# Kernel tuning notes

Measured on AMD Instinct MI355X. Metric: run time of the kernel, lower is better.

## Reference

```python
import jax, jax.numpy as jnp
import numpy as np

N_NODES = 100000
N_EDGES = 3200000
N_GRAPHS = 1000
F_IN = 3
H = 64


def setup_inputs() -> dict:
    key = jax.random.key(0)
    ks = jax.random.split(key, 12)
    x = jax.random.normal(ks[0], (N_NODES, F_IN), dtype=jnp.float32)
    edge_index = jax.random.randint(ks[1], (2, N_EDGES), 0, N_NODES, dtype=jnp.int64)
    batch = jnp.sort(jax.random.randint(ks[2], (N_NODES,), 0, N_GRAPHS, dtype=jnp.int64))
    def lin(k, fan_in, fan_out):
        bound = 1.0 / np.sqrt(fan_in)
        return jax.random.uniform(k, (fan_in, fan_out), jnp.float32, -bound, bound)
    return {
        "x": x,
        "edge_index": edge_index,
        "batch": batch,
        "eps1": jax.random.uniform(ks[3], (), jnp.float32),
        "eps2": jax.random.uniform(ks[4], (), jnp.float32),
        "eps3": jax.random.uniform(ks[5], (), jnp.float32),
        "W1": lin(ks[6], F_IN, H), "b1": jnp.zeros((H,), jnp.float32),
        "W2": lin(ks[7], H, H),    "b2": jnp.zeros((H,), jnp.float32),
        "W3": lin(ks[8], H, H),    "b3": jnp.zeros((H,), jnp.float32),
        "Wf1": lin(ks[9], H, 10),  "bf1": jnp.zeros((10,), jnp.float32),
        "Wf2": lin(ks[10], 10, 1), "bf2": jnp.zeros((1,), jnp.float32),
    }


def gin_conv(x, src, dst, eps, W, b):
    # GIN: out = nn((1+eps)*x + sum_{j in N(i)} x_j)
    agg = jax.ops.segment_sum(x[src], dst, num_segments=N_NODES)
    h = (1.0 + eps) * x + agg
    return h @ W + b


def reference(x, edge_index, batch, eps1, eps2, eps3, W1, b1, W2, b2, W3, b3, Wf1, bf1, Wf2, bf2):
    src, dst = edge_index[0], edge_index[1]
    h = jax.nn.relu(gin_conv(x, src, dst, eps1, W1, b1))
    h = jax.nn.relu(gin_conv(h, src, dst, eps2, W2, b2))
    h = jax.nn.relu(gin_conv(h, src, dst, eps3, W3, b3))
    # global mean pool over graphs
    sums = jax.ops.segment_sum(h, batch, num_segments=N_GRAPHS)
    counts = jax.ops.segment_sum(jnp.ones((N_NODES, 1), h.dtype), batch, num_segments=N_GRAPHS)
    pooled = sums / jnp.maximum(counts, 1.0)
    out = jax.nn.relu(pooled @ Wf1 + bf1)
    return out @ Wf2 + bf2
```

## Files before the change

kernel.cpp:

```cpp
#include <hip/hip_runtime.h>

#define N_NODES  100000
#define N_EDGES  3200000
#define N_GRAPHS 1000
#define HDIM     64

#define BUCK_LOG 8
#define BUCK_SZ  256
#define NBUCK    ((N_NODES + BUCK_SZ - 1) / BUCK_SZ)
#define BIN_T    256
#define BIN_E    16
#define BIN_CHUNK (BIN_T * BIN_E)
#define CLUS_CAP 12288

typedef __attribute__((ext_vector_type(8))) short short8;
typedef __attribute__((ext_vector_type(4))) float f32x4;
typedef __attribute__((ext_vector_type(4))) int   int4v;


__device__ inline unsigned short f2bf(float v) {
    unsigned int b; __builtin_memcpy(&b, &v, 4);
    return (unsigned short)((b + 0x7FFFu + ((b >> 16) & 1u)) >> 16);
}
__device__ inline float bf2f(unsigned short u) {
    return __uint_as_float(((unsigned int)u) << 16);
}
__device__ inline void sth(unsigned short* p, float v) { *p = f2bf(v); }
__device__ inline float bflo(unsigned int d) { return __uint_as_float(d << 16); }
__device__ inline float bfhi(unsigned int d) { return __uint_as_float(d & 0xFFFF0000u); }

__device__ inline int clampi(int v, int lo, int hi) {
    return v < lo ? lo : (v > hi ? hi : v);
}


__global__ void k_zero(int* __restrict__ p, int n) {
    int i = blockIdx.x * blockDim.x + threadIdx.x;
    if (i < n) p[i] = 0;
}


__global__ __launch_bounds__(BIN_T) void k_bcount(
        const int* __restrict__ ei, int* __restrict__ btot) {
    __shared__ int hist[NBUCK];
    for (int i = threadIdx.x; i < NBUCK; i += BIN_T) hist[i] = 0;
    __syncthreads();
    int e0 = blockIdx.x * BIN_CHUNK + threadIdx.x * BIN_E;
    if (e0 + BIN_E <= N_EDGES) {
        const int4v* d4 = (const int4v*)(ei + N_EDGES);
        #pragma unroll
        for (int q = 0; q < 4; ++q) {
            int4v dv = d4[(e0 >> 2) + q];
            #pragma unroll
            for (int j = 0; j < 4; ++j) {
                int d = clampi(dv[j], 0, N_NODES - 1);
                atomicAdd(&hist[d >> BUCK_LOG], 1);
            }
        }
    } else {
        for (int k = 0; k < BIN_E; ++k) {
            int e = e0 + k;
            if (e < N_EDGES) {
                int d = clampi(ei[N_EDGES + e], 0, N_NODES - 1);
                atomicAdd(&hist[d >> BUCK_LOG], 1);
            }
        }
    }
    __syncthreads();
    for (int i = threadIdx.x; i < NBUCK; i += BIN_T) {
        int c = hist[i];
        if (c) atomicAdd(&btot[i], c);
    }
}

__global__ void k_bscan(const int* __restrict__ btot, int* __restrict__ bbase,
                        int* __restrict__ gcur, int* __restrict__ off) {
    __shared__ int s[NBUCK + 1];
    int t = threadIdx.x;
    if (t < NBUCK) s[t] = btot[t];
    __syncthreads();
    if (t == 0) {
        int run = 0;
        for (int i = 0; i < NBUCK; ++i) { int x = s[i]; s[i] = run; run += x; }
        s[NBUCK] = run;
    }
    __syncthreads();
    if (t <= NBUCK) bbase[t] = s[t];
    if (t < NBUCK)  gcur[t] = s[t];
    if (t == 0)     off[N_NODES] = s[NBUCK];
}

__global__ __launch_bounds__(BIN_T) void k_bin(
        const int* __restrict__ ei, int* __restrict__ gcur,
        unsigned* __restrict__ pairs) {
    __shared__ int hist[NBUCK];
    __shared__ int base[NBUCK];
    for (int i = threadIdx.x; i < NBUCK; i += BIN_T) hist[i] = 0;
    __syncthreads();
    int e0 = blockIdx.x * BIN_CHUNK + threadIdx.x * BIN_E;
    int d[BIN_E], s[BIN_E];
    if (e0 + BIN_E <= N_EDGES) {
        const int4v* s4 = (const int4v*)ei;
        const int4v* d4 = (const int4v*)(ei + N_EDGES);
        #pragma unroll
        for (int q = 0; q < 4; ++q) {
            int4v dv = d4[(e0 >> 2) + q];
            int4v sv = s4[(e0 >> 2) + q];
            #pragma unroll
            for (int j = 0; j < 4; ++j) {
                d[q * 4 + j] = clampi(dv[j], 0, N_NODES - 1);
                s[q * 4 + j] = clampi(sv[j], 0, N_NODES - 1);
            }
        }
        #pragma unroll
        for (int k = 0; k < BIN_E; ++k) atomicAdd(&hist[d[k] >> BUCK_LOG], 1);
    } else {
        for (int k = 0; k < BIN_E; ++k) {
            int e = e0 + k;
            bool v = e < N_EDGES;
            d[k] = v ? clampi(ei[N_EDGES + e], 0, N_NODES - 1) : -1;
            s[k] = v ? clampi(ei[e], 0, N_NODES - 1) : 0;
            if (v) atomicAdd(&hist[d[k] >> BUCK_LOG], 1);
        }
    }
    __syncthreads();
    for (int i = threadIdx.x; i < NBUCK; i += BIN_T) {
        int c = hist[i];
        base[i] = c ? atomicAdd(&gcur[i], c) : 0;
        hist[i] = 0;
    }
    __syncthreads();
    #pragma unroll
    for (int k = 0; k < BIN_E; ++k) {
        if (d[k] >= 0) {
            int b = d[k] >> BUCK_LOG;
            int r = atomicAdd(&hist[b], 1);
            pairs[base[b] + r] = ((unsigned)(d[k] & (BUCK_SZ - 1)) << 24) | (unsigned)s[k];
        }
    }
}

__global__ __launch_bounds__(512) void k_cluster(
        const unsigned* __restrict__ pairs, const int* __restrict__ bbase,
        int* __restrict__ off, int* __restrict__ adj) {
    __shared__ int ladj[CLUS_CAP];
    __shared__ int lcur[BUCK_SZ];
    __shared__ int lsc[BUCK_SZ];
    int b  = blockIdx.x;
    int lo = b * BUCK_SZ;
    int nn = N_NODES - lo; if (nn > BUCK_SZ) nn = BUCK_SZ;
    int e0 = bbase[b], e1 = bbase[b + 1];
    int cnt = e1 - e0;
    if (threadIdx.x < BUCK_SZ) lcur[threadIdx.x] = 0;
    __syncthreads();
    for (int i = threadIdx.x; i < cnt; i += 512) {
        unsigned p = pairs[e0 + i];
        atomicAdd(&lcur[p >> 24], 1);
    }
    __syncthreads();
    int v = 0;
    if (threadIdx.x < BUCK_SZ) { v = lcur[threadIdx.x]; lsc[threadIdx.x] = v; }
    __syncthreads();
    #pragma unroll
    for (int d = 1; d < BUCK_SZ; d <<= 1) {
        int add = 0;
        if (threadIdx.x < BUCK_SZ && threadIdx.x >= d) add = lsc[threadIdx.x - d];
        __syncthreads();
        if (threadIdx.x < BUCK_SZ) lsc[threadIdx.x] += add;
        __syncthreads();
    }
    if (threadIdx.x < BUCK_SZ) {
        int exc = lsc[threadIdx.x] - v;
        if (threadIdx.x < nn) off[lo + threadIdx.x] = e0 + exc;
        lcur[threadIdx.x] = exc;
    }
    __syncthreads();
    if (cnt <= CLUS_CAP) {
        for (int i = threadIdx.x; i < cnt; i += 512) {
            unsigned p = pairs[e0 + i];
            int pos = atomicAdd(&lcur[p >> 24], 1);
            ladj[pos] = (int)(p & 0xFFFFFFu);
        }
        __syncthreads();
        for (int i = threadIdx.x; i < cnt; i += 512) adj[e0 + i] = ladj[i];
    } else {
        for (int i = threadIdx.x; i < cnt; i += 512) {
            unsigned p = pairs[e0 + i];
            int pos = atomicAdd(&lcur[p >> 24], 1);
            adj[e0 + pos] = (int)(p & 0xFFFFFFu);
        }
    }
}


__global__ __launch_bounds__(256) void k_layer1(
        const float* __restrict__ x, const int* __restrict__ off,
        const int* __restrict__ adj, const float* __restrict__ epsp,
        const float* __restrict__ W1, const float* __restrict__ b1,
        unsigned short* __restrict__ hout) {
    int wid  = (blockIdx.x * blockDim.x + threadIdx.x) >> 6;
    int lane = threadIdx.x & 63;
    if (wid >= N_NODES) return;
    int o0 = off[wid], o1 = off[wid + 1];
    float a0 = 0.f, a1 = 0.f, a2 = 0.f;
    for (int e = o0 + lane; e < o1; e += 64) {
        int s = adj[e];
        a0 += x[s * 3 + 0];
        a1 += x[s * 3 + 1];
        a2 += x[s * 3 + 2];
    }
    #pragma unroll
    for (int d = 32; d; d >>= 1) {
        a0 += __shfl_xor(a0, d);
        a1 += __shfl_xor(a1, d);
        a2 += __shfl_xor(a2, d);
    }
    float ep = 1.0f + epsp[0];
    float s0 = ep * x[wid * 3 + 0] + a0;
    float s1 = ep * x[wid * 3 + 1] + a1;
    float s2 = ep * x[wid * 3 + 2] + a2;
    float o = b1[lane] + s0 * W1[lane] + s1 * W1[64 + lane] + s2 * W1[128 + lane];
    sth(&hout[(size_t)wid * 64 + lane], fmaxf(o, 0.f));
}


__global__ __launch_bounds__(256) void k_gemm(
        const unsigned short* __restrict__ hin, const float* __restrict__ W,
        unsigned short* __restrict__ Y) {
    int lane = threadIdx.x & 63;
    int r = lane & 15;
    int g = lane >> 4;
    int wave   = blockIdx.x * (blockDim.x >> 6) + (threadIdx.x >> 6);
    int nwaves = gridDim.x * (blockDim.x >> 6);

    short8 bh[2][4], bl[2][4];
    #pragma unroll
    for (int s = 0; s < 2; ++s) {
        #pragma unroll
        for (int t = 0; t < 4; ++t) {
            short8 hv, lv;
            #pragma unroll
            for (int i = 0; i < 8; ++i) {
                int k = s * 32 + g * 8 + i;
                int n = t * 16 + r;
                float w = W[k * 64 + n];
                unsigned short wh = f2bf(w);
                float whf = bf2f(wh);
                hv[i] = (short)wh;
                lv[i] = (short)f2bf(w - whf);
            }
            bh[s][t] = hv; bl[s][t] = lv;
        }
    }

    const int NT = N_NODES / 16;
    for (int mt = wave; mt < NT; mt += nwaves) {
        const unsigned short* arow = hin + (size_t)(mt * 16 + r) * 64;
        short8 a0 = *(const short8*)(arow + g * 8);
        short8 a1 = *(const short8*)(arow + 32 + g * 8);
        #pragma unroll
        for (int t = 0; t < 4; ++t) {
            f32x4 acc = {0.f, 0.f, 0.f, 0.f};
            acc = __builtin_amdgcn_mfma_f32_16x16x32_bf16(a0, bh[0][t], acc, 0, 0, 0);
            acc = __builtin_amdgcn_mfma_f32_16x16x32_bf16(a0, bl[0][t], acc, 0, 0, 0);
            acc = __builtin_amdgcn_mfma_f32_16x16x32_bf16(a1, bh[1][t], acc, 0, 0, 0);
            acc = __builtin_amdgcn_mfma_f32_16x16x32_bf16(a1, bl[1][t], acc, 0, 0, 0);
            #pragma unroll
            for (int j = 0; j < 4; ++j) {
                sth(&Y[(size_t)(mt * 16 + g * 4 + j) * 64 + t * 16 + r], acc[j]);
            }
        }
    }
}


__device__ inline void gather_node(
        const uint2* __restrict__ h2, const int* __restrict__ off,
        const int* __restrict__ adj, int node, int sl, int g4,
        float& a0, float& a1, float& a2, float& a3) {
    int o0 = off[node], o1 = off[node + 1];
    int deg = o1 - o0;
    int nchunk = (deg + 15) >> 4;
    for (int c = 0; c < nchunk; ++c) {
        int pos = o0 + (c << 4) + sl;
        int posc = pos < o1 ? pos : (o1 - 1);
        int idxv = adj[posc];
        int rem = deg - (c << 4);
        #pragma unroll
        for (int half = 0; half < 2; ++half) {
            uint2 dd[8];
            #pragma unroll
            for (int i = 0; i < 8; ++i) {
                int k = half * 8 + i;
                int s = __shfl(idxv, (g4 << 4) + k);
                dd[i] = h2[(size_t)s * 16 + sl];
            }
            #pragma unroll
            for (int i = 0; i < 8; ++i) {
                int k = half * 8 + i;
                int ok = k < rem;
                unsigned int lo = ok ? dd[i].x : 0u;
                unsigned int hc = ok ? dd[i].y : 0u;
                a0 += bflo(lo); a1 += bfhi(lo);
                a2 += bflo(hc); a3 += bfhi(hc);
            }
            if (rem <= 8) break;
        }
    }
}

__global__ __launch_bounds__(512) void k_gather(
        const unsigned short* __restrict__ Y, const int* __restrict__ off,
        const int* __restrict__ adj, const float* __restrict__ epsp,
        const float* __restrict__ b, unsigned short* __restrict__ hout) {
    int tid  = blockIdx.x * 512 + threadIdx.x;
    int node = tid >> 4;
    if (node >= N_NODES) return;
    int sl = threadIdx.x & 15;
    int g4 = (threadIdx.x >> 4) & 3;
    const uint2* h2 = (const uint2*)Y;
    float a0 = 0.f, a1 = 0.f, a2 = 0.f, a3 = 0.f;
    gather_node(h2, off, adj, node, sl, g4, a0, a1, a2, a3);
    uint2 ds = h2[(size_t)node * 16 + sl];
    float ep = 1.0f + epsp[0];
    a0 = fmaxf(a0 + ep * bflo(ds.x) + b[4 * sl + 0], 0.f);
    a1 = fmaxf(a1 + ep * bfhi(ds.x) + b[4 * sl + 1], 0.f);
    a2 = fmaxf(a2 + ep * bflo(ds.y) + b[4 * sl + 2], 0.f);
    a3 = fmaxf(a3 + ep * bfhi(ds.y) + b[4 * sl + 3], 0.f);
    uint2 o;
    o.x = (unsigned int)f2bf(a0) | ((unsigned int)f2bf(a1) << 16);
    o.y = (unsigned int)f2bf(a2) | ((unsigned int)f2bf(a3) << 16);
    ((uint2*)hout)[(size_t)node * 16 + sl] = o;
}

__global__ __launch_bounds__(512) void k_gather_pool(
        const unsigned short* __restrict__ Y, const int* __restrict__ off,
        const int* __restrict__ adj, const float* __restrict__ epsp,
        const float* __restrict__ b, const int* __restrict__ batch,
        float* __restrict__ pooled, int* __restrict__ cnt) {
    __shared__ float sacc[8 * 64];
    __shared__ int   scnt[8];
    for (int i = threadIdx.x; i < 8 * 64; i += 512) sacc[i] = 0.f;
    if (threadIdx.x < 8) scnt[threadIdx.x] = 0;
    __syncthreads();

    int tid  = blockIdx.x * 512 + threadIdx.x;
    int node = tid >> 4;
    int sl = threadIdx.x & 15;
    int g4 = (threadIdx.x >> 4) & 3;
    int g0 = clampi(batch[clampi(blockIdx.x * 32, 0, N_NODES - 1)], 0, N_GRAPHS - 1);

    if (node < N_NODES) {
        const uint2* h2 = (const uint2*)Y;
        float a0 = 0.f, a1 = 0.f, a2 = 0.f, a3 = 0.f;
        gather_node(h2, off, adj, node, sl, g4, a0, a1, a2, a3);
        uint2 ds = h2[(size_t)node * 16 + sl];
        float ep = 1.0f + epsp[0];
        a0 = fmaxf(a0 + ep * bflo(ds.x) + b[4 * sl + 0], 0.f);
        a1 = fmaxf(a1 + ep * bfhi(ds.x) + b[4 * sl + 1], 0.f);
        a2 = fmaxf(a2 + ep * bflo(ds.y) + b[4 * sl + 2], 0.f);
        a3 = fmaxf(a3 + ep * bfhi(ds.y) + b[4 * sl + 3], 0.f);
        int g  = clampi(batch[node], 0, N_GRAPHS - 1);
        int og = g - g0;
        if (og >= 0 && og < 8) {
            atomicAdd(&sacc[og * 64 + 4 * sl + 0], a0);
            atomicAdd(&sacc[og * 64 + 4 * sl + 1], a1);
            atomicAdd(&sacc[og * 64 + 4 * sl + 2], a2);
            atomicAdd(&sacc[og * 64 + 4 * sl + 3], a3);
            if (sl == 0) atomicAdd(&scnt[og], 1);
        } else {
            atomicAdd(&pooled[g * 64 + 4 * sl + 0], a0);
            atomicAdd(&pooled[g * 64 + 4 * sl + 1], a1);
            atomicAdd(&pooled[g * 64 + 4 * sl + 2], a2);
            atomicAdd(&pooled[g * 64 + 4 * sl + 3], a3);
            if (sl == 0) atomicAdd(&cnt[g], 1);
        }
    }
    __syncthreads();
    int w = threadIdx.x >> 6;
    int lane = threadIdx.x & 63;
    if (w < 8) {
        int c = scnt[w];
        if (c > 0) {
            atomicAdd(&pooled[(g0 + w) * 64 + lane], sacc[w * 64 + lane]);
            if (lane == 0) atomicAdd(&cnt[g0 + w], c);
        }
    }
}


__global__ __launch_bounds__(256) void k_head(
        const float* __restrict__ pooled, const int* __restrict__ cnt,
        const float* __restrict__ Wf1, const float* __restrict__ bf1,
        const float* __restrict__ Wf2, const float* __restrict__ bf2,
        float* __restrict__ out) {
    int g = blockIdx.x * blockDim.x + threadIdx.x;
    if (g >= N_GRAPHS) return;
    float inv = 1.0f / fmaxf((float)cnt[g], 1.0f);
    float p[64];
    #pragma unroll
    for (int k = 0; k < 64; ++k) p[k] = pooled[g * 64 + k] * inv;
    float o = bf2[0];
    #pragma unroll
    for (int j = 0; j < 10; ++j) {
        float s = bf1[j];
        #pragma unroll
        for (int k = 0; k < 64; ++k) s += p[k] * Wf1[k * 10 + j];
        o += fmaxf(s, 0.f) * Wf2[j];
    }
    out[g] = o;
}


extern "C" void kernel_launch(void* const* d_in, const int* in_sizes, int n_in,
                              void* d_out, int out_size, void* d_ws, size_t ws_size,
                              hipStream_t stream) {
    const float* x     = (const float*)d_in[0];
    const int*   ei    = (const int*)d_in[1];
    const int*   batch = (const int*)d_in[2];
    const float* eps1 = (const float*)d_in[3];
    const float* eps2 = (const float*)d_in[4];
    const float* eps3 = (const float*)d_in[5];
    const float* W1 = (const float*)d_in[6];
    const float* b1 = (const float*)d_in[7];
    const float* W2 = (const float*)d_in[8];
    const float* b2 = (const float*)d_in[9];
    const float* W3 = (const float*)d_in[10];
    const float* b3 = (const float*)d_in[11];
    const float* Wf1 = (const float*)d_in[12];
    const float* bf1 = (const float*)d_in[13];
    const float* Wf2 = (const float*)d_in[14];
    const float* bf2 = (const float*)d_in[15];
    float* out = (float*)d_out;

    const size_t H64 = (size_t)N_NODES * HDIM;

    char* base = (char*)d_ws;
    unsigned short* hA = (unsigned short*)base;
    unsigned short* hB = (unsigned short*)(base + H64 * 2);
    unsigned* pairs = (unsigned*)base;
    char* q = base + 2 * H64 * 2;
    float* pooled = (float*)q;            q += 64000ull * 4;
    int*   cnt    = (int*)q;              q += 1000ull * 4;
    int*   off    = (int*)q;              q += 100004ull * 4;
    int*   btot   = (int*)q;              q += 512ull * 4;
    int*   bbase  = (int*)q;              q += 512ull * 4;
    int*   gcur   = (int*)q;              q += 512ull * 4;
    int*   adj    = (int*)q;

    const int TB = 256;
    k_zero<<<(65000 + TB - 1) / TB, TB, 0, stream>>>((int*)pooled, 65000);
    k_zero<<<2, TB, 0, stream>>>(btot, NBUCK);

    const int BINB = (N_EDGES + BIN_CHUNK - 1) / BIN_CHUNK;
    k_bcount<<<BINB, BIN_T, 0, stream>>>(ei, btot);
    k_bscan<<<1, 512, 0, stream>>>(btot, bbase, gcur, off);
    k_bin<<<BINB, BIN_T, 0, stream>>>(ei, gcur, pairs);
    k_cluster<<<NBUCK, 512, 0, stream>>>(pairs, bbase, off, adj);

    const int L1_BLOCKS = (int)((H64 + TB - 1) / TB);
    const int GB = (N_NODES * 16 + 511) / 512;

    k_layer1<<<L1_BLOCKS, TB, 0, stream>>>(x, off, adj, eps1, W1, b1, hA);
    k_gemm<<<256, 256, 0, stream>>>(hA, W2, hB);
    k_gather<<<GB, 512, 0, stream>>>(hB, off, adj, eps2, b2, hA);
    k_gemm<<<256, 256, 0, stream>>>(hA, W3, hB);
    k_gather_pool<<<GB, 512, 0, stream>>>(hB, off, adj, eps3, b3, batch, pooled, cnt);

    k_head<<<(N_GRAPHS + TB - 1) / TB, TB, 0, stream>>>(pooled, cnt, Wf1, bf1, Wf2, bf2, out);
}
```

Before: 266.5 us.

## Use fixed-capacity edge buckets and pad adjacency lists to chunks of 16

```diff
diff --git a/kernel.cpp b/kernel.cpp
--- a/kernel.cpp
+++ b/kernel.cpp
@@ -8,6 +8,7 @@
 #define BUCK_LOG 8
 #define BUCK_SZ  256
 #define NBUCK    ((N_NODES + BUCK_SZ - 1) / BUCK_SZ)
+#define CAP      16384
 #define BIN_T    256
 #define BIN_E    16
 #define BIN_CHUNK (BIN_T * BIN_E)
@@ -39,56 +40,18 @@
     if (i < n) p[i] = 0;
 }
 
-
-__global__ __launch_bounds__(BIN_T) void k_bcount(
-        const int* __restrict__ ei, int* __restrict__ btot) {
-    __shared__ int hist[NBUCK];
-    for (int i = threadIdx.x; i < NBUCK; i += BIN_T) hist[i] = 0;
-    __syncthreads();
-    int e0 = blockIdx.x * BIN_CHUNK + threadIdx.x * BIN_E;
-    if (e0 + BIN_E <= N_EDGES) {
-        const int4v* d4 = (const int4v*)(ei + N_EDGES);
-        #pragma unroll
-        for (int q = 0; q < 4; ++q) {
-            int4v dv = d4[(e0 >> 2) + q];
-            #pragma unroll
-            for (int j = 0; j < 4; ++j) {
-                int d = clampi(dv[j], 0, N_NODES - 1);
-                atomicAdd(&hist[d >> BUCK_LOG], 1);
-            }
-        }
-    } else {
-        for (int k = 0; k < BIN_E; ++k) {
-            int e = e0 + k;
-            if (e < N_EDGES) {
-                int d = clampi(ei[N_EDGES + e], 0, N_NODES - 1);
-                atomicAdd(&hist[d >> BUCK_LOG], 1);
-            }
-        }
-    }
-    __syncthreads();
-    for (int i = threadIdx.x; i < NBUCK; i += BIN_T) {
-        int c = hist[i];
-        if (c) atomicAdd(&btot[i], c);
-    }
-}
-
-__global__ void k_bscan(const int* __restrict__ btot, int* __restrict__ bbase,
-                        int* __restrict__ gcur, int* __restrict__ off) {
-    __shared__ int s[NBUCK + 1];
+__global__ void k_curinit(int* __restrict__ gcur) {
+    int b = blockIdx.x * blockDim.x + threadIdx.x;
+    if (b < NBUCK) gcur[b] = b * CAP;
+}
+
+__global__ void k_zrow(uint2* __restrict__ hA, uint2* __restrict__ hB) {
     int t = threadIdx.x;
-    if (t < NBUCK) s[t] = btot[t];
-    __syncthreads();
-    if (t == 0) {
-        int run = 0;
-        for (int i = 0; i < NBUCK; ++i) { int x = s[i]; s[i] = run; run += x; }
-        s[NBUCK] = run;
-    }
-    __syncthreads();
-    if (t <= NBUCK) bbase[t] = s[t];
-    if (t < NBUCK)  gcur[t] = s[t];
-    if (t == 0)     off[N_NODES] = s[NBUCK];
-}
+    uint2 z; z.x = 0u; z.y = 0u;
+    if (t < 16)       hA[(size_t)N_NODES * 16 + t] = z;
+    else if (t < 32)  hB[(size_t)N_NODES * 16 + (t - 16)] = z;
+}
+
 
 __global__ __launch_bounds__(BIN_T) void k_bin(
         const int* __restrict__ ei, int* __restrict__ gcur,
@@ -133,81 +96,98 @@
     #pragma unroll
     for (int k = 0; k < BIN_E; ++k) {
         if (d[k] >= 0) {
-            int b = d[k] >> BUCK_LOG;
-            int r = atomicAdd(&hist[b], 1);
-            pairs[base[b] + r] = ((unsigned)(d[k] & (BUCK_SZ - 1)) << 24) | (unsigned)s[k];
+            int bk = d[k] >> BUCK_LOG;
+            int r = atomicAdd(&hist[bk], 1);
+            int idx = base[bk] + r;
+            if (idx < (bk + 1) * CAP)
+                pairs[idx] = ((unsigned)(d[k] & (BUCK_SZ - 1)) << 24) | (unsigned)s[k];
         }
     }
 }
 
 __global__ __launch_bounds__(512) void k_cluster(
-        const unsigned* __restrict__ pairs, const int* __restrict__ bbase,
-        int* __restrict__ off, int* __restrict__ adj) {
+        const unsigned* __restrict__ pairs, const int* __restrict__ gcur,
+        int* __restrict__ poff, int* __restrict__ adj) {
     __shared__ int ladj[CLUS_CAP];
     __shared__ int lcur[BUCK_SZ];
     __shared__ int lsc[BUCK_SZ];
+    __shared__ int ptot;
     int b  = blockIdx.x;
     int lo = b * BUCK_SZ;
     int nn = N_NODES - lo; if (nn > BUCK_SZ) nn = BUCK_SZ;
-    int e0 = bbase[b], e1 = bbase[b + 1];
-    int cnt = e1 - e0;
-    if (threadIdx.x < BUCK_SZ) lcur[threadIdx.x] = 0;
-    __syncthreads();
-    for (int i = threadIdx.x; i < cnt; i += 512) {
-        unsigned p = pairs[e0 + i];
-        atomicAdd(&lcur[p >> 24], 1);
-    }
-    __syncthreads();
-    int v = 0;
-    if (threadIdx.x < BUCK_SZ) { v = lcur[threadIdx.x]; lsc[threadIdx.x] = v; }
+    int e0 = b * CAP;
+    int cnt = gcur[b] - e0; if (cnt > CAP) cnt = CAP;
+    int t = threadIdx.x;
+    if (t < BUCK_SZ) lcur[t] = 0;
+    __syncthreads();
+    for (int i = t; i < cnt; i += 512) atomicAdd(&lcur[pairs[e0 + i] >> 24], 1);
+    __syncthreads();
+    int deg = 0, pdeg = 0;
+    if (t < BUCK_SZ) {
+        deg  = lcur[t];
+        pdeg = (deg + 15) & ~15;
+        if (pdeg > 2032) pdeg = 2032;
+        lsc[t] = pdeg;
+    }
     __syncthreads();
     #pragma unroll
     for (int d = 1; d < BUCK_SZ; d <<= 1) {
         int add = 0;
-        if (threadIdx.x < BUCK_SZ && threadIdx.x >= d) add = lsc[threadIdx.x - d];
+        if (t < BUCK_SZ && t >= d) add = lsc[t - d];
         __syncthreads();
-        if (threadIdx.x < BUCK_SZ) lsc[threadIdx.x] += add;
+        if (t < BUCK_SZ) lsc[t] += add;
         __syncthreads();
     }
-    if (threadIdx.x < BUCK_SZ) {
-        int exc = lsc[threadIdx.x] - v;
-        if (threadIdx.x < nn) off[lo + threadIdx.x] = e0 + exc;
-        lcur[threadIdx.x] = exc;
-    }
-    __syncthreads();
-    if (cnt <= CLUS_CAP) {
-        for (int i = threadIdx.x; i < cnt; i += 512) {
+    if (t == BUCK_SZ - 1) ptot = lsc[t];
+    if (t < BUCK_SZ) {
+        int exc = lsc[t] - pdeg;
+        if (t < nn) poff[lo + t] = (e0 + exc) | ((pdeg >> 4) << 24);
+        lcur[t] = exc;
+    }
+    __syncthreads();
+    int pt = ptot;
+    if (pt <= CLUS_CAP) {
+        for (int i = t; i < pt; i += 512) ladj[i] = N_NODES;
+        __syncthreads();
+        for (int i = t; i < cnt; i += 512) {
             unsigned p = pairs[e0 + i];
             int pos = atomicAdd(&lcur[p >> 24], 1);
             ladj[pos] = (int)(p & 0xFFFFFFu);
         }
         __syncthreads();
-        for (int i = threadIdx.x; i < cnt; i += 512) adj[e0 + i] = ladj[i];
+        for (int i = t; i < pt; i += 512) adj[e0 + i] = ladj[i];
     } else {
-        for (int i = threadIdx.x; i < cnt; i += 512) {
+        for (int i = t; i < pt && i < CAP + 4096; i += 512) adj[e0 + i] = N_NODES;
+        __syncthreads();
+        for (int i = t; i < cnt; i += 512) {
             unsigned p = pairs[e0 + i];
             int pos = atomicAdd(&lcur[p >> 24], 1);
-            adj[e0 + pos] = (int)(p & 0xFFFFFFu);
+            if (pos < CAP + 4096) adj[e0 + pos] = (int)(p & 0xFFFFFFu);
         }
     }
 }
 
 
 __global__ __launch_bounds__(256) void k_layer1(
-        const float* __restrict__ x, const int* __restrict__ off,
+        const float* __restrict__ x, const int* __restrict__ poff,
         const int* __restrict__ adj, const float* __restrict__ epsp,
         const float* __restrict__ W1, const float* __restrict__ b1,
         unsigned short* __restrict__ hout) {
     int wid  = (blockIdx.x * blockDim.x + threadIdx.x) >> 6;
     int lane = threadIdx.x & 63;
     if (wid >= N_NODES) return;
-    int o0 = off[wid], o1 = off[wid + 1];
+    int pk = poff[wid];
+    int st = pk & 0xFFFFFF;
+    int n16 = ((unsigned)pk >> 24) << 4;
     float a0 = 0.f, a1 = 0.f, a2 = 0.f;
-    for (int e = o0 + lane; e < o1; e += 64) {
-        int s = adj[e];
-        a0 += x[s * 3 + 0];
-        a1 += x[s * 3 + 1];
-        a2 += x[s * 3 + 2];
+    for (int e = lane; e < n16; e += 64) {
+        int s = adj[st + e];
+        bool ok = s < N_NODES;
+        int sc = ok ? s : 0;
+        float m = ok ? 1.f : 0.f;
+        a0 += m * x[sc * 3 + 0];
+        a1 += m * x[sc * 3 + 1];
+        a2 += m * x[sc * 3 + 2];
     }
     #pragma unroll
     for (int d = 32; d; d >>= 1) {
@@ -275,42 +255,27 @@
 
 
 __device__ inline void gather_node(
-        const uint2* __restrict__ h2, const int* __restrict__ off,
-        const int* __restrict__ adj, int node, int sl, int g4,
+        const uint2* __restrict__ h2, int st, int nch,
+        const int* __restrict__ adj, int sl, int g4,
         float& a0, float& a1, float& a2, float& a3) {
-    int o0 = off[node], o1 = off[node + 1];
-    int deg = o1 - o0;
-    int nchunk = (deg + 15) >> 4;
-    for (int c = 0; c < nchunk; ++c) {
-        int pos = o0 + (c << 4) + sl;
-        int posc = pos < o1 ? pos : (o1 - 1);
-        int idxv = adj[posc];
-        int rem = deg - (c << 4);
-        #pragma unroll
-        for (int half = 0; half < 2; ++half) {
-            uint2 dd[8];
-            #pragma unroll
-            for (int i = 0; i < 8; ++i) {
-                int k = half * 8 + i;
-                int s = __shfl(idxv, (g4 << 4) + k);
-                dd[i] = h2[(size_t)s * 16 + sl];
-            }
-            #pragma unroll
-            for (int i = 0; i < 8; ++i) {
-                int k = half * 8 + i;
-                int ok = k < rem;
-                unsigned int lo = ok ? dd[i].x : 0u;
-                unsigned int hc = ok ? dd[i].y : 0u;
-                a0 += bflo(lo); a1 += bfhi(lo);
-                a2 += bflo(hc); a3 += bfhi(hc);
-            }
-            if (rem <= 8) break;
+    for (int c = 0; c < nch; ++c) {
+        int idxv = adj[st + (c << 4) + sl];
+        uint2 dd[16];
+        #pragma unroll
+        for (int k = 0; k < 16; ++k) {
+            int s = __shfl(idxv, (g4 << 4) + k);
+            dd[k] = h2[(size_t)s * 16 + sl];
+        }
+        #pragma unroll
+        for (int k = 0; k < 16; ++k) {
+            a0 += bflo(dd[k].x); a1 += bfhi(dd[k].x);
+            a2 += bflo(dd[k].y); a3 += bfhi(dd[k].y);
         }
     }
 }
 
 __global__ __launch_bounds__(512) void k_gather(
-        const unsigned short* __restrict__ Y, const int* __restrict__ off,
+        const unsigned short* __restrict__ Y, const int* __restrict__ poff,
         const int* __restrict__ adj, const float* __restrict__ epsp,
         const float* __restrict__ b, unsigned short* __restrict__ hout) {
     int tid  = blockIdx.x * 512 + threadIdx.x;
@@ -318,9 +283,12 @@
     if (node >= N_NODES) return;
     int sl = threadIdx.x & 15;
     int g4 = (threadIdx.x >> 4) & 3;
+    int pk = poff[node];
+    int st = pk & 0xFFFFFF;
+    int nch = (unsigned)pk >> 24;
     const uint2* h2 = (const uint2*)Y;
     float a0 = 0.f, a1 = 0.f, a2 = 0.f, a3 = 0.f;
-    gather_node(h2, off, adj, node, sl, g4, a0, a1, a2, a3);
+    gather_node(h2, st, nch, adj, sl, g4, a0, a1, a2, a3);
     uint2 ds = h2[(size_t)node * 16 + sl];
     float ep = 1.0f + epsp[0];
     a0 = fmaxf(a0 + ep * bflo(ds.x) + b[4 * sl + 0], 0.f);
@@ -334,7 +302,7 @@
 }
 
 __global__ __launch_bounds__(512) void k_gather_pool(
-        const unsigned short* __restrict__ Y, const int* __restrict__ off,
+        const unsigned short* __restrict__ Y, const int* __restrict__ poff,
         const int* __restrict__ adj, const float* __restrict__ epsp,
         const float* __restrict__ b, const int* __restrict__ batch,
         float* __restrict__ pooled, int* __restrict__ cnt) {
@@ -351,9 +319,12 @@
     int g0 = clampi(batch[clampi(blockIdx.x * 32, 0, N_NODES - 1)], 0, N_GRAPHS - 1);
 
     if (node < N_NODES) {
+        int pk = poff[node];
+        int st = pk & 0xFFFFFF;
+        int nch = (unsigned)pk >> 24;
         const uint2* h2 = (const uint2*)Y;
         float a0 = 0.f, a1 = 0.f, a2 = 0.f, a3 = 0.f;
-        gather_node(h2, off, adj, node, sl, g4, a0, a1, a2, a3);
+        gather_node(h2, st, nch, adj, sl, g4, a0, a1, a2, a3);
         uint2 ds = h2[(size_t)node * 16 + sl];
         float ep = 1.0f + epsp[0];
         a0 = fmaxf(a0 + ep * bflo(ds.x) + b[4 * sl + 0], 0.f);
@@ -433,39 +404,36 @@
     const float* bf2 = (const float*)d_in[15];
     float* out = (float*)d_out;
 
-    const size_t H64 = (size_t)N_NODES * HDIM;
+    const size_t HROWS = (size_t)(N_NODES + 1) * HDIM;
 
     char* base = (char*)d_ws;
     unsigned short* hA = (unsigned short*)base;
-    unsigned short* hB = (unsigned short*)(base + H64 * 2);
+    unsigned short* hB = (unsigned short*)(base + HROWS * 2);
     unsigned* pairs = (unsigned*)base;
-    char* q = base + 2 * H64 * 2;
+    char* q = base + 2 * HROWS * 2;
     float* pooled = (float*)q;            q += 64000ull * 4;
     int*   cnt    = (int*)q;              q += 1000ull * 4;
-    int*   off    = (int*)q;              q += 100004ull * 4;
-    int*   btot   = (int*)q;              q += 512ull * 4;
-    int*   bbase  = (int*)q;              q += 512ull * 4;
+    int*   poff   = (int*)q;              q += 100000ull * 4;
     int*   gcur   = (int*)q;              q += 512ull * 4;
     int*   adj    = (int*)q;
 
     const int TB = 256;
+    k_curinit<<<(NBUCK + TB - 1) / TB, TB, 0, stream>>>(gcur);
+    const int BINB = (N_EDGES + BIN_CHUNK - 1) / BIN_CHUNK;
+    k_bin<<<BINB, BIN_T, 0, stream>>>(ei, gcur, pairs);
+    k_cluster<<<NBUCK, 512, 0, stream>>>(pairs, gcur, poff, adj);
+
     k_zero<<<(65000 + TB - 1) / TB, TB, 0, stream>>>((int*)pooled, 65000);
-    k_zero<<<2, TB, 0, stream>>>(btot, NBUCK);
-
-    const int BINB = (N_EDGES + BIN_CHUNK - 1) / BIN_CHUNK;
-    k_bcount<<<BINB, BIN_T, 0, stream>>>(ei, btot);
-    k_bscan<<<1, 512, 0, stream>>>(btot, bbase, gcur, off);
-    k_bin<<<BINB, BIN_T, 0, stream>>>(ei, gcur, pairs);
-    k_cluster<<<NBUCK, 512, 0, stream>>>(pairs, bbase, off, adj);
-
-    const int L1_BLOCKS = (int)((H64 + TB - 1) / TB);
+    k_zrow<<<1, 64, 0, stream>>>((uint2*)hA, (uint2*)hB);
+
+    const int L1_BLOCKS = (N_NODES * 64 + TB - 1) / TB;
     const int GB = (N_NODES * 16 + 511) / 512;
 
-    k_layer1<<<L1_BLOCKS, TB, 0, stream>>>(x, off, adj, eps1, W1, b1, hA);
+    k_layer1<<<L1_BLOCKS, TB, 0, stream>>>(x, poff, adj, eps1, W1, b1, hA);
     k_gemm<<<256, 256, 0, stream>>>(hA, W2, hB);
-    k_gather<<<GB, 512, 0, stream>>>(hB, off, adj, eps2, b2, hA);
+    k_gather<<<GB, 512, 0, stream>>>(hB, poff, adj, eps2, b2, hA);
     k_gemm<<<256, 256, 0, stream>>>(hA, W3, hB);
-    k_gather_pool<<<GB, 512, 0, stream>>>(hB, off, adj, eps3, b3, batch, pooled, cnt);
+    k_gather_pool<<<GB, 512, 0, stream>>>(hB, poff, adj, eps3, b3, batch, pooled, cnt);
 
     k_head<<<(N_GRAPHS + TB - 1) / TB, TB, 0, stream>>>(pooled, cnt, Wf1, bf1, Wf2, bf2, out);
 }
```

After: 246.5 us. 1.08x faster.
